# Performance work log

Hardware: AMD Instinct MI355X
Metric: run time of the kernel (lower is better)

Reference implementation:

```python
import jax, jax.numpy as jnp
import numpy as np

D_MODEL = 1024
N_HEADS = 16
DEPTH = D_MODEL // N_HEADS
B, S = 2, 2048


def layer_norm(x, gamma, beta):
    # Faithful to the torch module: unbiased std (ddof=1), eps added to std.
    mean = jnp.mean(x, axis=-1, keepdims=True)
    std = jnp.std(x, axis=-1, ddof=1, keepdims=True)
    return gamma * ((x - mean) / (std + 1e-6)) + beta


def setup_inputs() -> dict:
    key = jax.random.key(0)
    ks = jax.random.split(key, 12)
    sc = 0.02
    x = jax.random.normal(ks[0], (B, S, D_MODEL), jnp.float32)
    mask = jnp.triu(jnp.ones((S, S), jnp.float32), k=1)  # 1 where masked (future)
    return {
        "x": x,
        "mask": mask,
        "wq_w": jax.random.normal(ks[1], (D_MODEL, D_MODEL), jnp.float32) * sc,
        "wq_b": jnp.zeros((D_MODEL,), jnp.float32),
        "wk_w": jax.random.normal(ks[2], (D_MODEL, D_MODEL), jnp.float32) * sc,
        "wk_b": jnp.zeros((D_MODEL,), jnp.float32),
        "wv_w": jax.random.normal(ks[3], (D_MODEL, D_MODEL), jnp.float32) * sc,
        "wv_b": jnp.zeros((D_MODEL,), jnp.float32),
        "dense_w": jax.random.normal(ks[4], (D_MODEL, D_MODEL), jnp.float32) * sc,
        "dense_b": jnp.zeros((D_MODEL,), jnp.float32),
        "gamma1": jnp.ones((D_MODEL,), jnp.float32),
        "beta1": jnp.zeros((D_MODEL,), jnp.float32),
        "gamma2": jnp.ones((D_MODEL,), jnp.float32),
        "beta2": jnp.zeros((D_MODEL,), jnp.float32),
        "fc_w": jax.random.normal(ks[5], (4 * D_MODEL, D_MODEL), jnp.float32) * sc,
        "proj_w": jax.random.normal(ks[6], (D_MODEL, 4 * D_MODEL), jnp.float32) * sc,
    }


def reference(x, mask, wq_w, wq_b, wk_w, wk_b, wv_w, wv_b, dense_w, dense_b,
              gamma1, beta1, gamma2, beta2, fc_w, proj_w):
    # x: [B,S,D]. Dropout is identity in eval.
    xn = layer_norm(x, gamma1, beta1)

    def split(h):  # [B,S,D] -> [B,H,S,depth]
        return h.reshape(B, S, N_HEADS, DEPTH).transpose(0, 2, 1, 3)

    q = split(xn @ wq_w.T + wq_b)
    k = split(xn @ wk_w.T + wk_b)
    v = split(xn @ wv_w.T + wv_b)

    scores = jnp.einsum("bhqd,bhkd->bhqk", q, k) / jnp.sqrt(
        jnp.asarray(DEPTH, jnp.float32))
    scores = scores + mask * -1e9
    attn = jax.nn.softmax(scores, axis=-1)
    ctx = jnp.einsum("bhqk,bhkd->bhqd", attn, v)
    ctx = ctx.transpose(0, 2, 1, 3).reshape(B, S, D_MODEL)
    attn_out = ctx @ dense_w.T + dense_b

    # Residual adds the *normed* x (faithful to the original ordering).
    h = xn + attn_out
    hn = layer_norm(h, gamma2, beta2)

    ff = jax.nn.gelu(hn @ fc_w.T, approximate=False) @ proj_w.T
    return hn + ff
```

## Files before the change

### kernel.cpp

```cpp
#include <hip/hip_runtime.h>
#include <math.h>

typedef __bf16 bf16;
typedef __attribute__((ext_vector_type(2))) __bf16 bf16x2;
typedef __attribute__((ext_vector_type(4))) __bf16 bf16x4;
typedef __attribute__((ext_vector_type(8))) __bf16 bf16x8;
typedef __attribute__((ext_vector_type(4))) float f32x4;

#define D_MODEL 1024
#define NH 16
#define DP 64
#define BB 2
#define SEQ 2048
#define TOK 4096
#define FFD 4096
#define AST 72

__device__ __forceinline__ void async16(bf16* lds, const bf16* g) {
    __builtin_amdgcn_global_load_lds(
        (__attribute__((address_space(1))) void*)g,
        (__attribute__((address_space(3))) void*)lds, 16, 0, 0);
}

__device__ __forceinline__ f32x4 mfma16(bf16x8 a, bf16x8 b, f32x4 c) {
    return __builtin_amdgcn_mfma_f32_16x16x32_bf16(a, b, c, 0, 0, 0);
}

__device__ __forceinline__ void xcd_swz(int& bx, int& by, int& bz) {
    const int gx = gridDim.x, gy = gridDim.y;
    const int nwg = gx * gy * gridDim.z;
    const int orig = (blockIdx.z * gy + blockIdx.y) * gx + blockIdx.x;
    const int q = nwg >> 3;
    const int n = (orig & 7) * q + (orig >> 3);
    bx = n % gx;
    const int r = n / gx;
    by = r % gy;
    bz = r / gy;
}

struct CvtArgs {
    const float4* in[6];
    bf16x4* out[6];
};
__global__ __launch_bounds__(256) void cvt_all(CvtArgs a)
{
    const int i = blockIdx.x * 256 + threadIdx.x;
    int seg, idx;
    if (i < (1 << 20)) { seg = i >> 18; idx = i & ((1 << 18) - 1); }
    else {
        const int j = i - (1 << 20);
        seg = 4 + (j >> 20); idx = j & ((1 << 20) - 1);
    }
    const float4 v = a.in[seg][idx];
    bf16x4 o; o[0] = (bf16)v.x; o[1] = (bf16)v.y; o[2] = (bf16)v.z; o[3] = (bf16)v.w;
    a.out[seg][idx] = o;
}

template<typename TIN>
__global__ __launch_bounds__(256) void ln_kernel(
    const TIN* __restrict__ in, const float* __restrict__ g,
    const float* __restrict__ be, bf16* __restrict__ out)
{
    const size_t row = blockIdx.x;
    const int t = threadIdx.x;
    const TIN* x = in + row * D_MODEL;

    float v0, v1, v2, v3;
    if constexpr (sizeof(TIN) == 4) {
        const float4 xv = *(const float4*)(x + t * 4);
        v0 = xv.x; v1 = xv.y; v2 = xv.z; v3 = xv.w;
    } else {
        const bf16x4 xv = *(const bf16x4*)(x + t * 4);
        v0 = (float)xv[0]; v1 = (float)xv[1]; v2 = (float)xv[2]; v3 = (float)xv[3];
    }
    float s  = v0 + v1 + v2 + v3;
    float ss = v0*v0 + v1*v1 + v2*v2 + v3*v3;
    #pragma unroll
    for (int off = 32; off > 0; off >>= 1) {
        s  += __shfl_down(s, off);
        ss += __shfl_down(ss, off);
    }
    __shared__ float rs[4], rss[4];
    if ((t & 63) == 0) { rs[t >> 6] = s; rss[t >> 6] = ss; }
    __syncthreads();
    const float S  = rs[0] + rs[1] + rs[2] + rs[3];
    const float SS = rss[0] + rss[1] + rss[2] + rss[3];
    const float mean = S * (1.0f / 1024.0f);
    const float var  = fmaxf((SS - S * mean) * (1.0f / 1023.0f), 0.0f);
    const float inv  = 1.0f / (sqrtf(var) + 1e-6f);

    const float4 gv = *(const float4*)(g  + t * 4);
    const float4 bv = *(const float4*)(be + t * 4);
    bf16x4 ov;
    ov[0] = (bf16)(gv.x * ((v0 - mean) * inv) + bv.x);
    ov[1] = (bf16)(gv.y * ((v1 - mean) * inv) + bv.y);
    ov[2] = (bf16)(gv.z * ((v2 - mean) * inv) + bv.z);
    ov[3] = (bf16)(gv.w * ((v3 - mean) * inv) + bv.w);
    *(bf16x4*)(out + row * D_MODEL + t * 4) = ov;
}

template<int EPI, typename TOUT>
__global__ __launch_bounds__(256, 2) void gemm_bt(
    const bf16* __restrict__ A, const bf16* __restrict__ W,
    const float* __restrict__ bias, const bf16* res,
    TOUT* C, int M, int N, int K, float scale)
{
    int bx, by, bz; xcd_swz(bx, by, bz);
    __shared__ __align__(16) bf16 As[2][128 * 32];
    __shared__ __align__(16) bf16 Bs[2][128 * 32];
    const int t = threadIdx.x;
    const int w = t >> 6, lane = t & 63;
    const int fr = lane & 15, quad = lane >> 4;
    const int m0 = by * 128, n0 = bx * 128;
    const int wm = (w >> 1) * 64, wn = (w & 1) * 64;

    const f32x4 z = {0.f, 0.f, 0.f, 0.f};
    f32x4 acc[4][4];
    #pragma unroll
    for (int i = 0; i < 4; ++i)
        #pragma unroll
        for (int j = 0; j < 4; ++j) acc[i][j] = z;

    const int nk = K >> 5;
    const int srow = t >> 2, ssub = t & 3;

    #pragma unroll
    for (int call = 0; call < 2; ++call) {
        const int row = call * 64 + srow;
        async16(&As[0][(size_t)(call * 256 + w * 64) * 8],
                A + (size_t)(m0 + row) * K + ssub * 8);
        async16(&Bs[0][(size_t)(call * 256 + w * 64) * 8],
                W + (size_t)(n0 + row) * K + ssub * 8);
    }
    __syncthreads();

    for (int kt = 0; kt < nk; ++kt) {
        const int cur = kt & 1;
        if (kt + 1 < nk) {
            const int k0 = (kt + 1) << 5;
            #pragma unroll
            for (int call = 0; call < 2; ++call) {
                const int row = call * 64 + srow;
                async16(&As[cur ^ 1][(size_t)(call * 256 + w * 64) * 8],
                        A + (size_t)(m0 + row) * K + k0 + ssub * 8);
                async16(&Bs[cur ^ 1][(size_t)(call * 256 + w * 64) * 8],
                        W + (size_t)(n0 + row) * K + k0 + ssub * 8);
            }
        }
        bf16x8 af[4], bfr[4];
        #pragma unroll
        for (int i = 0; i < 4; ++i)
            af[i] = *(const bf16x8*)&As[cur][(wm + i * 16 + fr) * 32 + quad * 8];
        #pragma unroll
        for (int j = 0; j < 4; ++j)
            bfr[j] = *(const bf16x8*)&Bs[cur][(wn + j * 16 + fr) * 32 + quad * 8];
        #pragma unroll
        for (int i = 0; i < 4; ++i)
            #pragma unroll
            for (int j = 0; j < 4; ++j)
                acc[i][j] = mfma16(af[i], bfr[j], acc[i][j]);
        __syncthreads();
    }

    #pragma unroll
    for (int i = 0; i < 4; ++i) {
        #pragma unroll
        for (int j = 0; j < 4; ++j) {
            #pragma unroll
            for (int r = 0; r < 4; ++r) {
                const int m = m0 + wm + i * 16 + quad * 4 + r;
                const int n = n0 + wn + j * 16 + fr;
                float v = acc[i][j][r];
                if (EPI == 1) {
                    v += bias[n];
                    v += (float)res[(size_t)m * N + n];
                    C[(size_t)m * N + n] = (TOUT)v;
                } else if (EPI == 2) {
                    v = 0.5f * v * (1.0f + erff(v * 0.70710678118f));
                    C[(size_t)m * N + n] = (TOUT)v;
                } else {
                    v += (float)res[(size_t)m * N + n];
                    C[(size_t)m * N + n] = (TOUT)v;
                }
            }
        }
    }
}

template<int EPI, typename TOUT>
__global__ __launch_bounds__(256, 2) void gemm_bt64(
    const bf16* __restrict__ A, const bf16* __restrict__ W,
    const float* __restrict__ bias, const bf16* res,
    TOUT* C, TOUT* Cb, int M, int N, int K, int kchunk)
{
    int bx, by, bz; xcd_swz(bx, by, bz);
    __shared__ __align__(16) bf16 As[2][128 * 32];
    __shared__ __align__(16) bf16 Bs[2][64 * 32];
    const int t = threadIdx.x;
    const int w = t >> 6, lane = t & 63;
    const int fr = lane & 15, quad = lane >> 4;
    const int m0 = by * 128, n0 = bx * 64;
    const int kbase = bz * kchunk;
    TOUT* Cz = (EPI == 4 && bz) ? Cb : C;
    const int wm = (w >> 1) * 64, wn = (w & 1) * 32;

    const f32x4 z = {0.f, 0.f, 0.f, 0.f};
    f32x4 acc[4][2];
    #pragma unroll
    for (int i = 0; i < 4; ++i)
        #pragma unroll
        for (int j = 0; j < 2; ++j) acc[i][j] = z;

    const int nk = kchunk >> 5;
    const int srow = t >> 2, ssub = t & 3;

    #pragma unroll
    for (int call = 0; call < 2; ++call) {
        const int row = call * 64 + srow;
        async16(&As[0][(size_t)(call * 256 + w * 64) * 8],
                A + (size_t)(m0 + row) * K + kbase + ssub * 8);
    }
    async16(&Bs[0][(size_t)(w * 64) * 8],
            W + (size_t)(n0 + srow) * K + kbase + ssub * 8);
    __syncthreads();

    for (int kt = 0; kt < nk; ++kt) {
        const int cur = kt & 1;
        if (kt + 1 < nk) {
            const int k0 = kbase + ((kt + 1) << 5);
            #pragma unroll
            for (int call = 0; call < 2; ++call) {
                const int row = call * 64 + srow;
                async16(&As[cur ^ 1][(size_t)(call * 256 + w * 64) * 8],
                        A + (size_t)(m0 + row) * K + k0 + ssub * 8);
            }
            async16(&Bs[cur ^ 1][(size_t)(w * 64) * 8],
                    W + (size_t)(n0 + srow) * K + k0 + ssub * 8);
        }
        bf16x8 af[4], bfr[2];
        #pragma unroll
        for (int i = 0; i < 4; ++i)
            af[i] = *(const bf16x8*)&As[cur][(wm + i * 16 + fr) * 32 + quad * 8];
        #pragma unroll
        for (int j = 0; j < 2; ++j)
            bfr[j] = *(const bf16x8*)&Bs[cur][(wn + j * 16 + fr) * 32 + quad * 8];
        #pragma unroll
        for (int i = 0; i < 4; ++i)
            #pragma unroll
            for (int j = 0; j < 2; ++j)
                acc[i][j] = mfma16(af[i], bfr[j], acc[i][j]);
        __syncthreads();
    }

    #pragma unroll
    for (int i = 0; i < 4; ++i) {
        #pragma unroll
        for (int j = 0; j < 2; ++j) {
            #pragma unroll
            for (int r = 0; r < 4; ++r) {
                const int m = m0 + wm + i * 16 + quad * 4 + r;
                const int n = n0 + wn + j * 16 + fr;
                float v = acc[i][j][r];
                if (EPI == 1) {
                    v += bias[n];
                    v += (float)res[(size_t)m * N + n];
                    Cz[(size_t)m * N + n] = (TOUT)v;
                } else if (EPI == 4) {
                    Cz[(size_t)m * N + n] = (TOUT)v;
                } else {
                    v += (float)res[(size_t)m * N + n];
                    Cz[(size_t)m * N + n] = (TOUT)v;
                }
            }
        }
    }
}

__global__ __launch_bounds__(256) void combine_add(
    const float4* __restrict__ p1, const bf16x4* __restrict__ res,
    float4* __restrict__ out)
{
    const int i = blockIdx.x * 256 + threadIdx.x;
    const float4 a = out[i], b = p1[i];
    const bf16x4 r = res[i];
    float4 o;
    o.x = a.x + b.x + (float)r[0];
    o.y = a.y + b.y + (float)r[1];
    o.z = a.z + b.z + (float)r[2];
    o.w = a.w + b.w + (float)r[3];
    out[i] = o;
}

__global__ __launch_bounds__(256, 2) void gemm_qkv(
    const bf16* __restrict__ A,
    const bf16* __restrict__ wq, const bf16* __restrict__ wk,
    const bf16* __restrict__ wvv,
    const float* __restrict__ bq, const float* __restrict__ bk,
    const float* __restrict__ bv,
    bf16* __restrict__ outq, bf16* __restrict__ outk, bf16* __restrict__ outv)
{
    int bx, by, bz; xcd_swz(bx, by, bz);
    const int sel = bx >> 3;
    const bf16* W = (sel == 0) ? wq : ((sel == 1) ? wk : wvv);
    const float* bias = (sel == 0) ? bq : ((sel == 1) ? bk : bv);
    bf16* C = (sel == 0) ? outq : ((sel == 1) ? outk : outv);
    const float scale = (sel == 0) ? 0.125f : 1.0f;
    const int K = D_MODEL;

    __shared__ __align__(16) bf16 As[2][128 * 32];
    __shared__ __align__(16) bf16 Bs[2][128 * 32];
    const int t = threadIdx.x;
    const int w = t >> 6, lane = t & 63;
    const int fr = lane & 15, quad = lane >> 4;
    const int m0 = by * 128, n0 = (bx & 7) * 128;
    const int wm = (w >> 1) * 64, wn = (w & 1) * 64;

    const f32x4 z = {0.f, 0.f, 0.f, 0.f};
    f32x4 acc[4][4];
    #pragma unroll
    for (int i = 0; i < 4; ++i)
        #pragma unroll
        for (int j = 0; j < 4; ++j) acc[i][j] = z;

    const int nk = D_MODEL >> 5;
    const int srow = t >> 2, ssub = t & 3;

    #pragma unroll
    for (int call = 0; call < 2; ++call) {
        const int row = call * 64 + srow;
        async16(&As[0][(size_t)(call * 256 + w * 64) * 8],
                A + (size_t)(m0 + row) * K + ssub * 8);
        async16(&Bs[0][(size_t)(call * 256 + w * 64) * 8],
                W + (size_t)(n0 + row) * K + ssub * 8);
    }
    __syncthreads();

    for (int kt = 0; kt < nk; ++kt) {
        const int cur = kt & 1;
        if (kt + 1 < nk) {
            const int k0 = (kt + 1) << 5;
            #pragma unroll
            for (int call = 0; call < 2; ++call) {
                const int row = call * 64 + srow;
                async16(&As[cur ^ 1][(size_t)(call * 256 + w * 64) * 8],
                        A + (size_t)(m0 + row) * K + k0 + ssub * 8);
                async16(&Bs[cur ^ 1][(size_t)(call * 256 + w * 64) * 8],
                        W + (size_t)(n0 + row) * K + k0 + ssub * 8);
            }
        }
        bf16x8 af[4], bfr[4];
        #pragma unroll
        for (int i = 0; i < 4; ++i)
            af[i] = *(const bf16x8*)&As[cur][(wm + i * 16 + fr) * 32 + quad * 8];
        #pragma unroll
        for (int j = 0; j < 4; ++j)
            bfr[j] = *(const bf16x8*)&Bs[cur][(wn + j * 16 + fr) * 32 + quad * 8];
        #pragma unroll
        for (int i = 0; i < 4; ++i)
            #pragma unroll
            for (int j = 0; j < 4; ++j)
                acc[i][j] = mfma16(af[i], bfr[j], acc[i][j]);
        __syncthreads();
    }

    #pragma unroll
    for (int i = 0; i < 4; ++i)
        #pragma unroll
        for (int j = 0; j < 4; ++j)
            #pragma unroll
            for (int r = 0; r < 4; ++r) {
                const int m = m0 + wm + i * 16 + quad * 4 + r;
                const int n = n0 + wn + j * 16 + fr;
                const float vv = (acc[i][j][r] + bias[n]) * scale;
                const int b = m >> 11, s = m & 2047, h = n >> 6, d = n & 63;
                C[(((size_t)(b * NH + h)) * SEQ + s) * DP + d] = (bf16)vv;
            }
}

__global__ __launch_bounds__(256, 2) void attn_kernel(
    const bf16* __restrict__ q, const bf16* __restrict__ k,
    const bf16* __restrict__ v, bf16* __restrict__ ctx)
{
    __shared__ __align__(16) bf16 Ks[2][64 * AST];
    __shared__ __align__(16) bf16 VsT[2][64 * AST];
    __shared__ __align__(16) bf16 Ps[4][16 * AST];
    const int t = threadIdx.x, wv = t >> 6, lane = t & 63;
    const int fr = lane & 15, quad = lane >> 4;
    const int id = blockIdx.y * 16 + blockIdx.x;
    const int nid = (id & 7) * 64 + (id >> 3);
    const int bh = nid >> 4;
    const int qxi = nid & 15;
    const size_t base = (size_t)bh * SEQ * DP;
    const int b = bh >> 4, hh = bh & 15;
    const f32x4 z = {0.f, 0.f, 0.f, 0.f};
    const int krow = t >> 2, kd0 = (t & 3) * 16;
    const int pp = t & 31, c0 = (t >> 5) * 8;

    for (int half = 0; half < 2; ++half) {
        const int qt = half ? (31 - qxi) : qxi;
        const int q0 = qt * 64, qr0 = q0 + wv * 16;
        const int nkt = qt + 1;

        __syncthreads();

        bf16x8 qf[2];
        #pragma unroll
        for (int c = 0; c < 2; ++c)
            qf[c] = *(const bf16x8*)(q + base + (size_t)(qr0 + fr) * DP + c * 32 + quad * 8);

        bf16x8 k0r, k1r, v0r, v1r;
        {
            const bf16* kp = k + base + (size_t)krow * DP + kd0;
            k0r = *(const bf16x8*)kp; k1r = *(const bf16x8*)(kp + 8);
            const bf16* vp = v + base + (size_t)(2 * pp) * DP + c0;
            v0r = *(const bf16x8*)vp; v1r = *(const bf16x8*)(vp + DP);
        }

        f32x4 o[4] = {z, z, z, z};
        float mi[4] = {-1e30f, -1e30f, -1e30f, -1e30f};
        float li[4] = {0.f, 0.f, 0.f, 0.f};

        for (int kt = 0; kt < nkt; ++kt) {
            const int cur = kt & 1;
            const int kk0 = kt * 64;
            *(bf16x8*)&Ks[cur][krow * AST + kd0]     = k0r;
            *(bf16x8*)&Ks[cur][krow * AST + kd0 + 8] = k1r;
            #pragma unroll
            for (int j = 0; j < 8; ++j) {
                bf16x2 pr; pr[0] = v0r[j]; pr[1] = v1r[j];
                *(bf16x2*)&VsT[cur][(c0 + j) * AST + 2 * pp] = pr;
            }
            __syncthreads();
            if (kt + 1 < nkt) {
                const bf16* kp = k + base + (size_t)(kk0 + 64 + krow) * DP + kd0;
                k0r = *(const bf16x8*)kp; k1r = *(const bf16x8*)(kp + 8);
                const bf16* vp = v + base + (size_t)(kk0 + 64 + 2 * pp) * DP + c0;
                v0r = *(const bf16x8*)vp; v1r = *(const bf16x8*)(vp + DP);
            }

            f32x4 sa[4] = {z, z, z, z};
            __builtin_amdgcn_s_setprio(1);
            #pragma unroll
            for (int nb = 0; nb < 4; ++nb)
                #pragma unroll
                for (int c = 0; c < 2; ++c) {
                    const bf16x8 kf = *(const bf16x8*)&Ks[cur][(nb * 16 + fr) * AST + c * 32 + quad * 8];
                    sa[nb] = mfma16(qf[c], kf, sa[nb]);
                }
            __builtin_amdgcn_s_setprio(0);

            float p[4][4], rmax[4];
            #pragma unroll
            for (int r = 0; r < 4; ++r) rmax[r] = -1e30f;
            #pragma unroll
            for (int nb = 0; nb < 4; ++nb)
                #pragma unroll
                for (int r = 0; r < 4; ++r) {
                    const int key = kk0 + nb * 16 + fr;
                    const int qrow = qr0 + quad * 4 + r;
                    float sv = sa[nb][r];
                    if (key > qrow) sv += -1e9f;
                    p[nb][r] = sv;
                    rmax[r] = fmaxf(rmax[r], sv);
                }
            #pragma unroll
            for (int off = 1; off < 16; off <<= 1)
                #pragma unroll
                for (int r = 0; r < 4; ++r)
                    rmax[r] = fmaxf(rmax[r], __shfl_xor(rmax[r], off));

            float alpha[4], psum[4];
            #pragma unroll
            for (int r = 0; r < 4; ++r) {
                const float nm = fmaxf(mi[r], rmax[r]);
                alpha[r] = __expf(mi[r] - nm);
                mi[r] = nm;
                float ps = 0.f;
                #pragma unroll
                for (int nb = 0; nb < 4; ++nb) {
                    const float e = __expf(p[nb][r] - nm);
                    p[nb][r] = e;
                    ps += e;
                }
                psum[r] = ps;
            }
            #pragma unroll
            for (int off = 1; off < 16; off <<= 1)
                #pragma unroll
                for (int r = 0; r < 4; ++r)
                    psum[r] += __shfl_xor(psum[r], off);
            #pragma unroll
            for (int r = 0; r < 4; ++r) li[r] = li[r] * alpha[r] + psum[r];
            #pragma unroll
            for (int db = 0; db < 4; ++db)
                #pragma unroll
                for (int r = 0; r < 4; ++r) o[db][r] *= alpha[r];

            #pragma unroll
            for (int nb = 0; nb < 4; ++nb)
                #pragma unroll
                for (int r = 0; r < 4; ++r)
                    Ps[wv][(quad * 4 + r) * AST + nb * 16 + fr] = (bf16)p[nb][r];

            bf16x8 pf[2];
            #pragma unroll
            for (int c = 0; c < 2; ++c)
                pf[c] = *(const bf16x8*)&Ps[wv][fr * AST + c * 32 + quad * 8];
            __builtin_amdgcn_s_setprio(1);
            #pragma unroll
            for (int db = 0; db < 4; ++db)
                #pragma unroll
                for (int c = 0; c < 2; ++c) {
                    const bf16x8 vf = *(const bf16x8*)&VsT[cur][(db * 16 + fr) * AST + c * 32 + quad * 8];
                    o[db] = mfma16(pf[c], vf, o[db]);
                }
            __builtin_amdgcn_s_setprio(0);
        }

        #pragma unroll
        for (int db = 0; db < 4; ++db)
            #pragma unroll
            for (int r = 0; r < 4; ++r) {
                const int qrow = qr0 + quad * 4 + r;
                const int d = db * 16 + fr;
                ctx[((size_t)(b * SEQ + qrow)) * D_MODEL + hh * DP + d] =
                    (bf16)(o[db][r] / li[r]);
            }
    }
}

extern "C" void kernel_launch(void* const* d_in, const int* in_sizes, int n_in,
                              void* d_out, int out_size, void* d_ws, size_t ws_size,
                              hipStream_t stream) {
    const float* x       = (const float*)d_in[0];
    const float* wq_w    = (const float*)d_in[2];
    const float* wq_b    = (const float*)d_in[3];
    const float* wk_w    = (const float*)d_in[4];
    const float* wk_b    = (const float*)d_in[5];
    const float* wv_w    = (const float*)d_in[6];
    const float* wv_b    = (const float*)d_in[7];
    const float* dense_w = (const float*)d_in[8];
    const float* dense_b = (const float*)d_in[9];
    const float* gamma1  = (const float*)d_in[10];
    const float* beta1   = (const float*)d_in[11];
    const float* gamma2  = (const float*)d_in[12];
    const float* beta2   = (const float*)d_in[13];
    const float* fc_w    = (const float*)d_in[14];
    const float* proj_w  = (const float*)d_in[15];
    float* out = (float*)d_out;

    bf16* ws = (bf16*)d_ws;
    const size_t M1 = (size_t)1 << 20;
    bf16* xn   = ws;
    bf16* qb   = ws + 4 * M1;
    bf16* kb   = ws + 8 * M1;
    bf16* vb   = ws + 12 * M1;
    bf16* ctx  = ws + 16 * M1;
    bf16* ff1  = qb;
    bf16* wqc  = ws + 20 * M1;
    bf16* wkc  = ws + 21 * M1;
    bf16* wvc  = ws + 22 * M1;
    bf16* wdc  = ws + 23 * M1;
    bf16* fcc  = ws + 24 * M1;
    bf16* prjc = ws + 28 * M1;
    bf16* h = xn, *hn = xn;
    float* part1 = (float*)(ws + 20 * M1);

    CvtArgs ca;
    ca.in[0] = (const float4*)wq_w;    ca.out[0] = (bf16x4*)wqc;
    ca.in[1] = (const float4*)wk_w;    ca.out[1] = (bf16x4*)wkc;
    ca.in[2] = (const float4*)wv_w;    ca.out[2] = (bf16x4*)wvc;
    ca.in[3] = (const float4*)dense_w; ca.out[3] = (bf16x4*)wdc;
    ca.in[4] = (const float4*)fc_w;    ca.out[4] = (bf16x4*)fcc;
    ca.in[5] = (const float4*)proj_w;  ca.out[5] = (bf16x4*)prjc;
    cvt_all<<<12288, 256, 0, stream>>>(ca);

    ln_kernel<float><<<TOK, 256, 0, stream>>>(x, gamma1, beta1, xn);
    gemm_qkv<<<dim3(24, 32), 256, 0, stream>>>(xn, wqc, wkc, wvc,
                                               wq_b, wk_b, wv_b, qb, kb, vb);
    attn_kernel<<<dim3(16, BB * NH), 256, 0, stream>>>(qb, kb, vb, ctx);
    gemm_bt64<1, bf16><<<dim3(16, 32), 256, 0, stream>>>(
        ctx, wdc, dense_b, xn, h, (bf16*)nullptr, TOK, D_MODEL, D_MODEL, D_MODEL);
    ln_kernel<bf16><<<TOK, 256, 0, stream>>>(h, gamma2, beta2, hn);
    gemm_bt<2, bf16><<<dim3(32, 32), 256, 0, stream>>>(hn, fcc, nullptr, nullptr, ff1,
                                                       TOK, FFD, D_MODEL, 1.0f);
    gemm_bt64<4, float><<<dim3(16, 32, 2), 256, 0, stream>>>(
        ff1, prjc, nullptr, nullptr, out, part1, TOK, D_MODEL, FFD, FFD / 2);
    combine_add<<<4096, 256, 0, stream>>>(
        (const float4*)part1, (const bf16x4*)hn, (float4*)out);
}
```

Baseline: 382.0 us.

## Split attention into one block per query tile with transposed S layout

```diff
diff --git a/kernel.cpp b/kernel.cpp
--- a/kernel.cpp
+++ b/kernel.cpp
@@ -377,7 +377,7 @@
             }
 }
 
-__global__ __launch_bounds__(256, 2) void attn_kernel(
+__global__ __launch_bounds__(256, 3) void attn_kernel(
     const bf16* __restrict__ q, const bf16* __restrict__ k,
     const bf16* __restrict__ v, bf16* __restrict__ ctx)
 {
@@ -386,147 +386,139 @@
     __shared__ __align__(16) bf16 Ps[4][16 * AST];
     const int t = threadIdx.x, wv = t >> 6, lane = t & 63;
     const int fr = lane & 15, quad = lane >> 4;
-    const int id = blockIdx.y * 16 + blockIdx.x;
-    const int nid = (id & 7) * 64 + (id >> 3);
-    const int bh = nid >> 4;
-    const int qxi = nid & 15;
+    const int id = blockIdx.y * 32 + blockIdx.x;
+    const int nid = (id & 7) * 128 + (id >> 3);
+    const int bh = nid >> 5;
+    const int qt = 31 - (nid & 31);
     const size_t base = (size_t)bh * SEQ * DP;
     const int b = bh >> 4, hh = bh & 15;
     const f32x4 z = {0.f, 0.f, 0.f, 0.f};
     const int krow = t >> 2, kd0 = (t & 3) * 16;
     const int pp = t & 31, c0 = (t >> 5) * 8;
 
-    for (int half = 0; half < 2; ++half) {
-        const int qt = half ? (31 - qxi) : qxi;
-        const int q0 = qt * 64, qr0 = q0 + wv * 16;
-        const int nkt = qt + 1;
-
+    const int q0 = qt * 64, qr0 = q0 + wv * 16;
+    const int nkt = qt + 1;
+    const int myq = qr0 + fr;
+
+    bf16x8 qf[2];
+    #pragma unroll
+    for (int c = 0; c < 2; ++c)
+        qf[c] = *(const bf16x8*)(q + base + (size_t)myq * DP + c * 32 + quad * 8);
+
+    bf16x8 k0r, k1r, v0r, v1r;
+    {
+        const bf16* kp = k + base + (size_t)krow * DP + kd0;
+        k0r = *(const bf16x8*)kp; k1r = *(const bf16x8*)(kp + 8);
+        const bf16* vp = v + base + (size_t)(2 * pp) * DP + c0;
+        v0r = *(const bf16x8*)vp; v1r = *(const bf16x8*)(vp + DP);
+    }
+
+    f32x4 o[4] = {z, z, z, z};
+    float mi = -1e30f, li = 0.f;
+
+    for (int kt = 0; kt < nkt; ++kt) {
+        const int cur = kt & 1;
+        const int kk0 = kt * 64;
+        *(bf16x8*)&Ks[cur][krow * AST + kd0]     = k0r;
+        *(bf16x8*)&Ks[cur][krow * AST + kd0 + 8] = k1r;
+        #pragma unroll
+        for (int j = 0; j < 8; ++j) {
+            bf16x2 pr; pr[0] = v0r[j]; pr[1] = v1r[j];
+            *(bf16x2*)&VsT[cur][(c0 + j) * AST + 2 * pp] = pr;
+        }
         __syncthreads();
-
-        bf16x8 qf[2];
+        if (kt + 1 < nkt) {
+            const bf16* kp = k + base + (size_t)(kk0 + 64 + krow) * DP + kd0;
+            k0r = *(const bf16x8*)kp; k1r = *(const bf16x8*)(kp + 8);
+            const bf16* vp = v + base + (size_t)(kk0 + 64 + 2 * pp) * DP + c0;
+            v0r = *(const bf16x8*)vp; v1r = *(const bf16x8*)(vp + DP);
+        }
+
+        f32x4 sa[4] = {z, z, z, z};
+        __builtin_amdgcn_s_setprio(1);
+        #pragma unroll
+        for (int nb = 0; nb < 4; ++nb)
+            #pragma unroll
+            for (int c = 0; c < 2; ++c) {
+                const bf16x8 kf = *(const bf16x8*)&Ks[cur][(nb * 16 + fr) * AST + c * 32 + quad * 8];
+                sa[nb] = mfma16(kf, qf[c], sa[nb]);
+            }
+        __builtin_amdgcn_s_setprio(0);
+
+        float p[4][4];
+        float rmax = -1e30f;
+        #pragma unroll
+        for (int nb = 0; nb < 4; ++nb)
+            #pragma unroll
+            for (int r = 0; r < 4; ++r) {
+                const int key = kk0 + nb * 16 + quad * 4 + r;
+                float sv = sa[nb][r];
+                if (key > myq) sv += -1e9f;
+                p[nb][r] = sv;
+                rmax = fmaxf(rmax, sv);
+            }
+        rmax = fmaxf(rmax, __shfl_xor(rmax, 16));
+        rmax = fmaxf(rmax, __shfl_xor(rmax, 32));
+
+        const float nm = fmaxf(mi, rmax);
+        const float alpha = __expf(mi - nm);
+        mi = nm;
+        float ps = 0.f;
+        #pragma unroll
+        for (int nb = 0; nb < 4; ++nb)
+            #pragma unroll
+            for (int r = 0; r < 4; ++r) {
+                const float e = __expf(p[nb][r] - nm);
+                p[nb][r] = e;
+                ps += e;
+            }
+        ps += __shfl_xor(ps, 16);
+        ps += __shfl_xor(ps, 32);
+        li = li * alpha + ps;
+
+        float ab[4];
+        #pragma unroll
+        for (int r = 0; r < 4; ++r) ab[r] = __shfl(alpha, quad * 4 + r, 16);
+        #pragma unroll
+        for (int db = 0; db < 4; ++db)
+            #pragma unroll
+            for (int r = 0; r < 4; ++r) o[db][r] *= ab[r];
+
+        #pragma unroll
+        for (int nb = 0; nb < 4; ++nb) {
+            bf16x4 pw;
+            pw[0] = (bf16)p[nb][0]; pw[1] = (bf16)p[nb][1];
+            pw[2] = (bf16)p[nb][2]; pw[3] = (bf16)p[nb][3];
+            *(bf16x4*)&Ps[wv][fr * AST + nb * 16 + quad * 4] = pw;
+        }
+
+        bf16x8 pf[2];
         #pragma unroll
         for (int c = 0; c < 2; ++c)
-            qf[c] = *(const bf16x8*)(q + base + (size_t)(qr0 + fr) * DP + c * 32 + quad * 8);
-
-        bf16x8 k0r, k1r, v0r, v1r;
-        {
-            const bf16* kp = k + base + (size_t)krow * DP + kd0;
-            k0r = *(const bf16x8*)kp; k1r = *(const bf16x8*)(kp + 8);
-            const bf16* vp = v + base + (size_t)(2 * pp) * DP + c0;
-            v0r = *(const bf16x8*)vp; v1r = *(const bf16x8*)(vp + DP);
-        }
-
-        f32x4 o[4] = {z, z, z, z};
-        float mi[4] = {-1e30f, -1e30f, -1e30f, -1e30f};
-        float li[4] = {0.f, 0.f, 0.f, 0.f};
-
-        for (int kt = 0; kt < nkt; ++kt) {
-            const int cur = kt & 1;
-            const int kk0 = kt * 64;
-            *(bf16x8*)&Ks[cur][krow * AST + kd0]     = k0r;
-            *(bf16x8*)&Ks[cur][krow * AST + kd0 + 8] = k1r;
-            #pragma unroll
-            for (int j = 0; j < 8; ++j) {
-                bf16x2 pr; pr[0] = v0r[j]; pr[1] = v1r[j];
-                *(bf16x2*)&VsT[cur][(c0 + j) * AST + 2 * pp] = pr;
-            }
-            __syncthreads();
-            if (kt + 1 < nkt) {
-                const bf16* kp = k + base + (size_t)(kk0 + 64 + krow) * DP + kd0;
-                k0r = *(const bf16x8*)kp; k1r = *(const bf16x8*)(kp + 8);
-                const bf16* vp = v + base + (size_t)(kk0 + 64 + 2 * pp) * DP + c0;
-                v0r = *(const bf16x8*)vp; v1r = *(const bf16x8*)(vp + DP);
-            }
-
-            f32x4 sa[4] = {z, z, z, z};
-            __builtin_amdgcn_s_setprio(1);
-            #pragma unroll
-            for (int nb = 0; nb < 4; ++nb)
-                #pragma unroll
-                for (int c = 0; c < 2; ++c) {
-                    const bf16x8 kf = *(const bf16x8*)&Ks[cur][(nb * 16 + fr) * AST + c * 32 + quad * 8];
-                    sa[nb] = mfma16(qf[c], kf, sa[nb]);
-                }
-            __builtin_amdgcn_s_setprio(0);
-
-            float p[4][4], rmax[4];
-            #pragma unroll
-            for (int r = 0; r < 4; ++r) rmax[r] = -1e30f;
-            #pragma unroll
-            for (int nb = 0; nb < 4; ++nb)
-                #pragma unroll
-                for (int r = 0; r < 4; ++r) {
-                    const int key = kk0 + nb * 16 + fr;
-                    const int qrow = qr0 + quad * 4 + r;
-                    float sv = sa[nb][r];
-                    if (key > qrow) sv += -1e9f;
-                    p[nb][r] = sv;
-                    rmax[r] = fmaxf(rmax[r], sv);
-                }
-            #pragma unroll
-            for (int off = 1; off < 16; off <<= 1)
-                #pragma unroll
-                for (int r = 0; r < 4; ++r)
-                    rmax[r] = fmaxf(rmax[r], __shfl_xor(rmax[r], off));
-
-            float alpha[4], psum[4];
-            #pragma unroll
-            for (int r = 0; r < 4; ++r) {
-                const float nm = fmaxf(mi[r], rmax[r]);
-                alpha[r] = __expf(mi[r] - nm);
-                mi[r] = nm;
-                float ps = 0.f;
-                #pragma unroll
-                for (int nb = 0; nb < 4; ++nb) {
-                    const float e = __expf(p[nb][r] - nm);
-                    p[nb][r] = e;
-                    ps += e;
-                }
-                psum[r] = ps;
-            }
-            #pragma unroll
-            for (int off = 1; off < 16; off <<= 1)
-                #pragma unroll
-                for (int r = 0; r < 4; ++r)
-                    psum[r] += __shfl_xor(psum[r], off);
-            #pragma unroll
-            for (int r = 0; r < 4; ++r) li[r] = li[r] * alpha[r] + psum[r];
-            #pragma unroll
-            for (int db = 0; db < 4; ++db)
-                #pragma unroll
-                for (int r = 0; r < 4; ++r) o[db][r] *= alpha[r];
-
-            #pragma unroll
-            for (int nb = 0; nb < 4; ++nb)
-                #pragma unroll
-                for (int r = 0; r < 4; ++r)
-                    Ps[wv][(quad * 4 + r) * AST + nb * 16 + fr] = (bf16)p[nb][r];
-
-            bf16x8 pf[2];
-            #pragma unroll
-            for (int c = 0; c < 2; ++c)
-                pf[c] = *(const bf16x8*)&Ps[wv][fr * AST + c * 32 + quad * 8];
-            __builtin_amdgcn_s_setprio(1);
-            #pragma unroll
-            for (int db = 0; db < 4; ++db)
-                #pragma unroll
-                for (int c = 0; c < 2; ++c) {
-                    const bf16x8 vf = *(const bf16x8*)&VsT[cur][(db * 16 + fr) * AST + c * 32 + quad * 8];
-                    o[db] = mfma16(pf[c], vf, o[db]);
-                }
-            __builtin_amdgcn_s_setprio(0);
-        }
-
+            pf[c] = *(const bf16x8*)&Ps[wv][fr * AST + c * 32 + quad * 8];
+        __builtin_amdgcn_s_setprio(1);
         #pragma unroll
         for (int db = 0; db < 4; ++db)
             #pragma unroll
-            for (int r = 0; r < 4; ++r) {
-                const int qrow = qr0 + quad * 4 + r;
-                const int d = db * 16 + fr;
-                ctx[((size_t)(b * SEQ + qrow)) * D_MODEL + hh * DP + d] =
-                    (bf16)(o[db][r] / li[r]);
-            }
-    }
+            for (int c = 0; c < 2; ++c) {
+                const bf16x8 vf = *(const bf16x8*)&VsT[cur][(db * 16 + fr) * AST + c * 32 + quad * 8];
+                o[db] = mfma16(pf[c], vf, o[db]);
+            }
+        __builtin_amdgcn_s_setprio(0);
+    }
+
+    float lir[4];
+    #pragma unroll
+    for (int r = 0; r < 4; ++r) lir[r] = __shfl(li, quad * 4 + r, 16);
+    #pragma unroll
+    for (int db = 0; db < 4; ++db)
+        #pragma unroll
+        for (int r = 0; r < 4; ++r) {
+            const int qrow = qr0 + quad * 4 + r;
+            const int d = db * 16 + fr;
+            ctx[((size_t)(b * SEQ + qrow)) * D_MODEL + hh * DP + d] =
+                (bf16)(o[db][r] / lir[r]);
+        }
 }
 
 extern "C" void kernel_launch(void* const* d_in, const int* in_sizes, int n_in,
@@ -578,7 +570,7 @@
     ln_kernel<float><<<TOK, 256, 0, stream>>>(x, gamma1, beta1, xn);
     gemm_qkv<<<dim3(24, 32), 256, 0, stream>>>(xn, wqc, wkc, wvc,
                                                wq_b, wk_b, wv_b, qb, kb, vb);
-    attn_kernel<<<dim3(16, BB * NH), 256, 0, stream>>>(qb, kb, vb, ctx);
+    attn_kernel<<<dim3(32, BB * NH), 256, 0, stream>>>(qb, kb, vb, ctx);
     gemm_bt64<1, bf16><<<dim3(16, 32), 256, 0, stream>>>(
         ctx, wdc, dense_b, xn, h, (bf16*)nullptr, TOK, D_MODEL, D_MODEL, D_MODEL);
     ln_kernel<bf16><<<TOK, 256, 0, stream>>>(h, gamma2, beta2, hn);
```

Measured after the change: 375.8 us. About the same (-1.6%).
